# Kernel tuning notes

Hardware: AMD Instinct MI355X
Metric: run time of the kernel (lower is better)

The kernel has to match this reference:

```python
import jax, jax.numpy as jnp
import numpy as np

NUM_HEADS = 16
NHID = 64
D = NUM_HEADS * NHID  # 1024, also keys/query/values dim and out_dim
SL, BS = 2048, 32


def setup_inputs() -> dict:
    key = jax.random.key(0)
    ks = jax.random.split(key, 7)
    s = 1.0 / np.sqrt(D)
    return {
        "query": jax.random.normal(ks[0], (BS, D), jnp.float32),
        "keys": jax.random.normal(ks[1], (SL, BS, D), jnp.float32),
        "values": jax.random.normal(ks[2], (SL, BS, D), jnp.float32),
        "Wq": jax.random.normal(ks[3], (D, D), jnp.float32) * s,
        "Wk": jax.random.normal(ks[4], (D, D), jnp.float32) * s,
        "Wv": jax.random.normal(ks[5], (D, D), jnp.float32) * s,
        "Wo": jax.random.normal(ks[6], (D, D), jnp.float32) * s,
    }


def reference(query, keys, values, Wq, Wk, Wv, Wo):
    sl, bs, _ = keys.shape
    qp = query @ Wq.T                       # [bs, H*nhid]
    kp = keys @ Wk.T                        # [sl, bs, H*nhid]
    vp = values @ Wv.T                      # [sl, bs, H*nhid]
    # elementwise multiplicative score, reduced per head
    dot = (qp * kp).reshape(sl, bs, NUM_HEADS, NHID).sum(-1) / np.sqrt(NHID)
    # NOTE: original uses log_softmax (not softmax) over the sequence dim
    w = jax.nn.log_softmax(dot, axis=0)[..., None]        # [sl, bs, H, 1]
    attn = (w * vp.reshape(sl, bs, NUM_HEADS, NHID)).sum(0)  # [bs, H, nhid]
    return attn.reshape(bs, -1) @ Wo.T                     # [bs, D]
```

## Files before the change

kernel.cpp:

```cpp
#include <hip/hip_runtime.h>

#define SL  2048
#define BSZ 32
#define DIM 1024
#define NH  16
#define HD  64

typedef __attribute__((ext_vector_type(4))) float f32x4;
typedef __attribute__((ext_vector_type(8))) short s16x8;

static __device__ __forceinline__ short f2bf(float f) {
    union { float f; unsigned u; } v; v.f = f;
    unsigned r = (v.u + 0x7fffu + ((v.u >> 16) & 1u)) >> 16;
    return (short)r;
}

__global__ __launch_bounds__(256) void k_qu(const float* __restrict__ query,
                                            const float* __restrict__ Wq,
                                            const float* __restrict__ Wk,
                                            short* __restrict__ u) {
    int b = blockIdx.x & 31;
    int h = blockIdx.x >> 5;
    int t = threadIdx.x;
    __shared__ float red[256];
    __shared__ float sq[HD];
    {
        int i  = t >> 2;
        int kq = t & 3;
        const float* q = query + (size_t)b * DIM + kq * 256;
        const float* w = Wq + (size_t)(h * HD + i) * DIM + kq * 256;
        f32x4 acc = {0.f, 0.f, 0.f, 0.f};
#pragma unroll 4
        for (int k = 0; k < 256; k += 4)
            acc += *(const f32x4*)(q + k) * *(const f32x4*)(w + k);
        red[t] = acc[0] + acc[1] + acc[2] + acc[3];
    }
    __syncthreads();
    if (t < HD) sq[t] = (red[t*4] + red[t*4+1] + red[t*4+2] + red[t*4+3]) * 0.125f;
    __syncthreads();
    f32x4 acc = {0.f, 0.f, 0.f, 0.f};
    const float* wk = Wk + (size_t)(h * HD) * DIM;
#pragma unroll 8
    for (int i = 0; i < HD; ++i) {
        float s = sq[i];
        const float* row = wk + (size_t)i * DIM;
        acc[0] += s * row[t];
        acc[1] += s * row[t + 256];
        acc[2] += s * row[t + 512];
        acc[3] += s * row[t + 768];
    }
    short* ub = u + ((size_t)(b * NH + h)) * DIM;
    ub[t]       = f2bf(acc[0]);
    ub[t + 256] = f2bf(acc[1]);
    ub[t + 512] = f2bf(acc[2]);
    ub[t + 768] = f2bf(acc[3]);
}

__global__ __launch_bounds__(256, 4) void k_dot(const float* __restrict__ keys,
                                                const short* __restrict__ u,
                                                float* __restrict__ dot,
                                                float2* __restrict__ part) {
    int b  = blockIdx.x & 31;
    int st = blockIdx.x >> 5;
    int s0 = st * 64;
    __shared__ short ulds[NH][DIM + 8];
    {
        const uint4* src = (const uint4*)(u + (size_t)b * NH * DIM);
        for (int idx = threadIdx.x; idx < NH * DIM / 8; idx += 256) {
            int row = idx >> 7;
            int col = (idx & 127) * 8;
            *(uint4*)&ulds[row][col] = src[idx];
        }
    }
    __syncthreads();
    int lane = threadIdx.x & 63;
    int wave = threadIdx.x >> 6;
    int lrow = lane & 15;
    int kgrp = lane >> 4;
    f32x4 acc = {0.f, 0.f, 0.f, 0.f};
    const float* ka = keys + ((size_t)(s0 + wave * 16 + lrow) * BSZ + b) * DIM;
#pragma unroll 4
    for (int k0 = 0; k0 < DIM; k0 += 32) {
        int kj = k0 + kgrp * 8;
        s16x8 bf = *(const s16x8*)&ulds[lrow][kj];
        f32x4 a0 = *(const f32x4*)(ka + kj);
        f32x4 a1 = *(const f32x4*)(ka + kj + 4);
        s16x8 af;
        af[0]=f2bf(a0[0]); af[1]=f2bf(a0[1]); af[2]=f2bf(a0[2]); af[3]=f2bf(a0[3]);
        af[4]=f2bf(a1[0]); af[5]=f2bf(a1[1]); af[6]=f2bf(a1[2]); af[7]=f2bf(a1[3]);
        acc = __builtin_amdgcn_mfma_f32_16x16x32_bf16(af, bf, acc, 0, 0, 0);
    }
    size_t obase = ((size_t)b * SL + (s0 + wave * 16 + kgrp * 4)) * NH + lrow;
#pragma unroll
    for (int r = 0; r < 4; ++r)
        dot[obase + (size_t)r * NH] = acc[r];

    __shared__ float mred[4][16], lred[4][16];
    float m = fmaxf(fmaxf(acc[0], acc[1]), fmaxf(acc[2], acc[3]));
    m = fmaxf(m, __shfl_xor(m, 16));
    m = fmaxf(m, __shfl_xor(m, 32));
    if (lane < 16) mred[wave][lrow] = m;
    __syncthreads();
    float mb = fmaxf(fmaxf(mred[0][lrow], mred[1][lrow]),
                     fmaxf(mred[2][lrow], mred[3][lrow]));
    float l = __expf(acc[0]-mb) + __expf(acc[1]-mb) + __expf(acc[2]-mb) + __expf(acc[3]-mb);
    l += __shfl_xor(l, 16);
    l += __shfl_xor(l, 32);
    if (lane < 16) lred[wave][lrow] = l;
    __syncthreads();
    int t = threadIdx.x;
    if (t < 16) {
        float mbb = fmaxf(fmaxf(mred[0][t], mred[1][t]), fmaxf(mred[2][t], mred[3][t]));
        float lb  = lred[0][t] + lred[1][t] + lred[2][t] + lred[3][t];
        part[((size_t)b * 32 + st) * 16 + t] = make_float2(mbb, lb);
    }
}

__global__ __launch_bounds__(256, 4) void k_z(const float* __restrict__ values,
                                              const float* __restrict__ w,
                                              const float2* __restrict__ part,
                                              float* __restrict__ z) {
    int x  = blockIdx.x;
    int b  = x & 31;
    int jc = (x >> 5) & 15;
    int sh = x >> 9;
    int t  = threadIdx.x;
    int ssub = t >> 4;
    int jq = t & 15;
    int j = jc * 64 + jq * 4;
    int wv = __builtin_amdgcn_readfirstlane(t >> 6);
    int lane = t & 63;

    __shared__ float wlds[128 * 16];
    __shared__ float Tl[16];
    __shared__ f32x4 redW[4][16][16];
    __shared__ f32x4 redV[4][16];

    if (t < 16) {
        const float2* pb = part + (size_t)b * 32 * 16 + t;
        float M = -1e30f;
#pragma unroll
        for (int i = 0; i < 32; ++i) M = fmaxf(M, pb[i * 16].x);
        float L = 0.f;
#pragma unroll
        for (int i = 0; i < 32; ++i) { float2 p = pb[i * 16]; L += p.y * __expf(p.x - M); }
        Tl[t] = M + __logf(L);
    }

    f32x4 acc[NH];
#pragma unroll
    for (int h = 0; h < NH; ++h) acc[h] = (f32x4){0.f,0.f,0.f,0.f};
    f32x4 accV = {0.f,0.f,0.f,0.f};

    const float* vbase = values + (size_t)b * DIM + j;
    const float* wbase = w + ((size_t)b * SL + sh * 1024) * NH;

    const f32x4* src = (const f32x4*)wbase;
    f32x4 w0 = src[t], w1 = src[t + 256];

    for (int ph = 0; ph < 8; ++ph) {
        __syncthreads();
        f32x4* dst = (f32x4*)wlds;
        dst[t]       = w0;
        dst[t + 256] = w1;
        __syncthreads();
        if (ph + 1 < 8) {
            src += 512;
            w0 = src[t];
            w1 = src[t + 256];
        }
        int sbase = sh * 1024 + ph * 128;
#pragma unroll 4
        for (int it = 0; it < 8; ++it) {
            int s_loc = it * 16 + ssub;
            f32x4 v = *(const f32x4*)(vbase + (size_t)(sbase + s_loc) * (BSZ * DIM));
            const f32x4* wr = (const f32x4*)(wlds + s_loc * 16);
            f32x4 wv0 = wr[0], wv1 = wr[1], wv2 = wr[2], wv3 = wr[3];
            acc[0]  += v * wv0[0]; acc[1]  += v * wv0[1]; acc[2]  += v * wv0[2]; acc[3]  += v * wv0[3];
            acc[4]  += v * wv1[0]; acc[5]  += v * wv1[1]; acc[6]  += v * wv1[2]; acc[7]  += v * wv1[3];
            acc[8]  += v * wv2[0]; acc[9]  += v * wv2[1]; acc[10] += v * wv2[2]; acc[11] += v * wv2[3];
            acc[12] += v * wv3[0]; acc[13] += v * wv3[1]; acc[14] += v * wv3[2]; acc[15] += v * wv3[3];
            accV += v;
        }
    }

#pragma unroll
    for (int h = 0; h < NH; ++h) {
#pragma unroll
        for (int e = 0; e < 4; ++e) {
            float x0 = acc[h][e];
            x0 += __shfl_xor(x0, 16);
            x0 += __shfl_xor(x0, 32);
            acc[h][e] = x0;
        }
    }
#pragma unroll
    for (int e = 0; e < 4; ++e) {
        float x0 = accV[e];
        x0 += __shfl_xor(x0, 16);
        x0 += __shfl_xor(x0, 32);
        accV[e] = x0;
    }
    if (lane < 16) {
#pragma unroll
        for (int h = 0; h < NH; ++h) redW[wv][h][lane] = acc[h];
        redV[wv][lane] = accV;
    }
    __syncthreads();
    int h2 = t >> 4, q = t & 15;
    f32x4 sumW = redW[0][h2][q] + redW[1][h2][q] + redW[2][h2][q] + redW[3][h2][q];
    f32x4 sumV = redV[0][q] + redV[1][q] + redV[2][q] + redV[3][q];
    float Th = Tl[h2];
    f32x4 zv = sumW - Th * sumV;
    float* zp = z + (size_t)sh * (BSZ * NH * DIM);
    *(f32x4*)(zp + ((size_t)(b * NH + h2)) * DIM + jc * 64 + q * 4) = zv;
}

template<bool DUAL>
__global__ __launch_bounds__(256) void k_gemm(const float* __restrict__ A,
                                              const float* __restrict__ A2,
                                              const float* __restrict__ W,
                                              float* __restrict__ O,
                                              int rmul, int hsel) {
    int oc = blockIdx.x & 15;
    int b  = blockIdx.x >> 4;
    int wv = __builtin_amdgcn_readfirstlane(threadIdx.x >> 6);
    int lane = threadIdx.x & 63;
    int o = oc * 64 + lane;
    int row = b * rmul + (hsel ? oc : 0);
    const float* arow  = A + (size_t)row * DIM + wv * 256;
    const float* a2row = DUAL ? (A2 + (size_t)row * DIM + wv * 256) : nullptr;
    const float* wrow  = W + (size_t)o * DIM + wv * 256;
    f32x4 acc = {0.f, 0.f, 0.f, 0.f};
#pragma unroll 4
    for (int k = 0; k < 256; k += 4) {
        f32x4 a = *(const f32x4*)(arow + k);
        if (DUAL) a += *(const f32x4*)(a2row + k);
        f32x4 w = *(const f32x4*)(wrow + k);
        acc += a * w;
    }
    __shared__ float red[4][64];
    red[wv][lane] = acc[0] + acc[1] + acc[2] + acc[3];
    __syncthreads();
    int t = threadIdx.x;
    if (t < 64)
        O[(size_t)b * DIM + oc * 64 + t] = red[0][t] + red[1][t] + red[2][t] + red[3][t];
}

extern "C" void kernel_launch(void* const* d_in, const int* in_sizes, int n_in,
                              void* d_out, int out_size, void* d_ws, size_t ws_size,
                              hipStream_t stream) {
    const float* query  = (const float*)d_in[0];
    const float* keys   = (const float*)d_in[1];
    const float* values = (const float*)d_in[2];
    const float* Wq = (const float*)d_in[3];
    const float* Wk = (const float*)d_in[4];
    const float* Wv = (const float*)d_in[5];
    const float* Wo = (const float*)d_in[6];
    float* out = (float*)d_out;

    char* ws = (char*)d_ws;
    short*  u    = (short*)(ws + 0);
    float*  dotb = (float*)(ws + (1 << 20));
    float*  z0   = (float*)(ws + (5 << 20));
    float*  z1   = (float*)(ws + (7 << 20));
    float*  attn = (float*)(ws + (9 << 20));
    float2* part = (float2*)(ws + (9 << 20) + (128 << 10));

    hipLaunchKernelGGL(k_qu,          dim3(512),  dim3(256), 0, stream, query, Wq, Wk, u);
    hipLaunchKernelGGL(k_dot,         dim3(1024), dim3(256), 0, stream, keys, u, dotb, part);
    hipLaunchKernelGGL(k_z,           dim3(1024), dim3(256), 0, stream, values, dotb, part, z0);
    hipLaunchKernelGGL(k_gemm<true>,  dim3(512),  dim3(256), 0, stream, z0, z1, Wv, attn, 16, 1);
    hipLaunchKernelGGL(k_gemm<false>, dim3(512),  dim3(256), 0, stream, attn, nullptr, Wo, out, 1, 0);
}
```

Before: 229.4 us.

## Parallelize softmax partial reduction and drop register prefetch of weight tiles

The per-head log-sum-exp merge of 32 partials now runs in two stages: 128 threads each merge 4 partials, then 16 threads combine the 8 results through shared memory, replacing the serial 32-step loop done by 16 threads. The register double-buffered prefetch of weight tiles is removed, so each phase loads its tile directly from global memory into LDS, which lowers register pressure at the cost of exposing the load latency. The inner loop reads weights as scalars from LDS instead of four vector loads, leaving the load width to the compiler.

```diff
diff --git a/kernel.cpp b/kernel.cpp
--- a/kernel.cpp
+++ b/kernel.cpp
@@ -133,17 +133,28 @@
 
     __shared__ float wlds[128 * 16];
     __shared__ float Tl[16];
+    __shared__ float mred8[8][16], lred8[8][16];
     __shared__ f32x4 redW[4][16][16];
     __shared__ f32x4 redV[4][16];
 
+    if (t < 128) {
+        int h = t & 15, g = t >> 4;
+        const float2* pb = part + (size_t)b * 32 * 16 + h;
+        float2 p0 = pb[(g*4+0)*16], p1 = pb[(g*4+1)*16],
+               p2 = pb[(g*4+2)*16], p3 = pb[(g*4+3)*16];
+        float M = fmaxf(fmaxf(p0.x, p1.x), fmaxf(p2.x, p3.x));
+        float L = p0.y*__expf(p0.x-M) + p1.y*__expf(p1.x-M)
+                + p2.y*__expf(p2.x-M) + p3.y*__expf(p3.x-M);
+        mred8[g][h] = M; lred8[g][h] = L;
+    }
+    __syncthreads();
     if (t < 16) {
-        const float2* pb = part + (size_t)b * 32 * 16 + t;
-        float M = -1e30f;
-#pragma unroll
-        for (int i = 0; i < 32; ++i) M = fmaxf(M, pb[i * 16].x);
+        float M = mred8[0][t];
+#pragma unroll
+        for (int g = 1; g < 8; ++g) M = fmaxf(M, mred8[g][t]);
         float L = 0.f;
 #pragma unroll
-        for (int i = 0; i < 32; ++i) { float2 p = pb[i * 16]; L += p.y * __expf(p.x - M); }
+        for (int g = 0; g < 8; ++g) L += lred8[g][t] * __expf(mred8[g][t] - M);
         Tl[t] = M + __logf(L);
     }
 
@@ -155,31 +166,26 @@
     const float* vbase = values + (size_t)b * DIM + j;
     const float* wbase = w + ((size_t)b * SL + sh * 1024) * NH;
 
-    const f32x4* src = (const f32x4*)wbase;
-    f32x4 w0 = src[t], w1 = src[t + 256];
-
     for (int ph = 0; ph < 8; ++ph) {
         __syncthreads();
-        f32x4* dst = (f32x4*)wlds;
-        dst[t]       = w0;
-        dst[t + 256] = w1;
+        {
+            const f32x4* src = (const f32x4*)(wbase + ph * 128 * NH);
+            f32x4* dst = (f32x4*)wlds;
+            dst[t]       = src[t];
+            dst[t + 256] = src[t + 256];
+        }
         __syncthreads();
-        if (ph + 1 < 8) {
-            src += 512;
-            w0 = src[t];
-            w1 = src[t + 256];
-        }
         int sbase = sh * 1024 + ph * 128;
 #pragma unroll 4
         for (int it = 0; it < 8; ++it) {
             int s_loc = it * 16 + ssub;
             f32x4 v = *(const f32x4*)(vbase + (size_t)(sbase + s_loc) * (BSZ * DIM));
-            const f32x4* wr = (const f32x4*)(wlds + s_loc * 16);
-            f32x4 wv0 = wr[0], wv1 = wr[1], wv2 = wr[2], wv3 = wr[3];
-            acc[0]  += v * wv0[0]; acc[1]  += v * wv0[1]; acc[2]  += v * wv0[2]; acc[3]  += v * wv0[3];
-            acc[4]  += v * wv1[0]; acc[5]  += v * wv1[1]; acc[6]  += v * wv1[2]; acc[7]  += v * wv1[3];
-            acc[8]  += v * wv2[0]; acc[9]  += v * wv2[1]; acc[10] += v * wv2[2]; acc[11] += v * wv2[3];
-            acc[12] += v * wv3[0]; acc[13] += v * wv3[1]; acc[14] += v * wv3[2]; acc[15] += v * wv3[3];
+            const float* wr = wlds + s_loc * 16;
+#pragma unroll
+            for (int h = 0; h < NH; ++h) {
+                float wh = wr[h];
+                acc[h] += v * wh;
+            }
             accV += v;
         }
     }
```

New measurement: 207.9 us. 1.1x faster.

## Widen dot and z kernels to 512 threads, drop split-sequence z partials

Applied to the files above, without the earlier changes.

k_dot now processes 128 sequence rows per block with 8 waves, which halves the block count and the number of softmax partials. k_z no longer splits the sequence into two halves with separate z buffers. Each block instead covers the full sequence with 512 threads, each handling 2 columns instead of 4, and the DUAL sum in the first GEMM is removed. This cuts launch-level duplication and an extra z buffer pass, at the cost of longer per-block loops, fewer blocks, and the loss of the register-prefetch double buffering of the weights.

```diff
diff --git a/kernel.cpp b/kernel.cpp
--- a/kernel.cpp
+++ b/kernel.cpp
@@ -7,6 +7,7 @@
 #define HD  64
 
 typedef __attribute__((ext_vector_type(4))) float f32x4;
+typedef __attribute__((ext_vector_type(2))) float f32x2;
 typedef __attribute__((ext_vector_type(8))) short s16x8;
 
 static __device__ __forceinline__ short f2bf(float f) {
@@ -56,25 +57,29 @@
     ub[t + 768] = f2bf(acc[3]);
 }
 
-__global__ __launch_bounds__(256, 4) void k_dot(const float* __restrict__ keys,
+__global__ __launch_bounds__(512, 6) void k_dot(const float* __restrict__ keys,
                                                 const short* __restrict__ u,
                                                 float* __restrict__ dot,
                                                 float2* __restrict__ part) {
     int b  = blockIdx.x & 31;
     int st = blockIdx.x >> 5;
-    int s0 = st * 64;
+    int s0 = st * 128;
     __shared__ short ulds[NH][DIM + 8];
+    __shared__ float mred[8][16], lred[8][16];
+    int t = threadIdx.x;
     {
         const uint4* src = (const uint4*)(u + (size_t)b * NH * DIM);
-        for (int idx = threadIdx.x; idx < NH * DIM / 8; idx += 256) {
+#pragma unroll
+        for (int r = 0; r < 4; ++r) {
+            int idx = t + r * 512;
             int row = idx >> 7;
             int col = (idx & 127) * 8;
             *(uint4*)&ulds[row][col] = src[idx];
         }
     }
     __syncthreads();
-    int lane = threadIdx.x & 63;
-    int wave = threadIdx.x >> 6;
+    int lane = t & 63;
+    int wave = t >> 6;
     int lrow = lane & 15;
     int kgrp = lane >> 4;
     f32x4 acc = {0.f, 0.f, 0.f, 0.f};
@@ -95,91 +100,88 @@
     for (int r = 0; r < 4; ++r)
         dot[obase + (size_t)r * NH] = acc[r];
 
-    __shared__ float mred[4][16], lred[4][16];
     float m = fmaxf(fmaxf(acc[0], acc[1]), fmaxf(acc[2], acc[3]));
     m = fmaxf(m, __shfl_xor(m, 16));
     m = fmaxf(m, __shfl_xor(m, 32));
     if (lane < 16) mred[wave][lrow] = m;
     __syncthreads();
-    float mb = fmaxf(fmaxf(mred[0][lrow], mred[1][lrow]),
-                     fmaxf(mred[2][lrow], mred[3][lrow]));
+    float mb = mred[0][lrow];
+#pragma unroll
+    for (int w = 1; w < 8; ++w) mb = fmaxf(mb, mred[w][lrow]);
     float l = __expf(acc[0]-mb) + __expf(acc[1]-mb) + __expf(acc[2]-mb) + __expf(acc[3]-mb);
     l += __shfl_xor(l, 16);
     l += __shfl_xor(l, 32);
     if (lane < 16) lred[wave][lrow] = l;
     __syncthreads();
-    int t = threadIdx.x;
     if (t < 16) {
-        float mbb = fmaxf(fmaxf(mred[0][t], mred[1][t]), fmaxf(mred[2][t], mred[3][t]));
-        float lb  = lred[0][t] + lred[1][t] + lred[2][t] + lred[3][t];
-        part[((size_t)b * 32 + st) * 16 + t] = make_float2(mbb, lb);
-    }
-}
-
-__global__ __launch_bounds__(256, 4) void k_z(const float* __restrict__ values,
-                                              const float* __restrict__ w,
+        float mbb = mred[0][t];
+#pragma unroll
+        for (int w = 1; w < 8; ++w) mbb = fmaxf(mbb, mred[w][t]);
+        float lb = lred[0][t];
+#pragma unroll
+        for (int w = 1; w < 8; ++w) lb += lred[w][t];
+        part[((size_t)b * 16 + st) * 16 + t] = make_float2(mbb, lb);
+    }
+}
+
+__global__ __launch_bounds__(512, 6) void k_z(const float* __restrict__ values,
+                                              const float* __restrict__ dotb,
                                               const float2* __restrict__ part,
                                               float* __restrict__ z) {
-    int x  = blockIdx.x;
-    int b  = x & 31;
-    int jc = (x >> 5) & 15;
-    int sh = x >> 9;
+    int b  = blockIdx.x & 31;
+    int jc = blockIdx.x >> 5;
     int t  = threadIdx.x;
-    int ssub = t >> 4;
-    int jq = t & 15;
-    int j = jc * 64 + jq * 4;
-    int wv = __builtin_amdgcn_readfirstlane(t >> 6);
+    int ssub = t >> 5;
+    int jq   = t & 31;
+    int wave = t >> 6;
     int lane = t & 63;
 
     __shared__ float wlds[128 * 16];
     __shared__ float Tl[16];
-    __shared__ f32x4 redW[4][16][16];
-    __shared__ f32x4 redV[4][16];
+    __shared__ f32x2 redW[8][16][32];
+    __shared__ f32x2 redV[8][32];
 
     if (t < 16) {
-        const float2* pb = part + (size_t)b * 32 * 16 + t;
+        const float2* pb = part + (size_t)b * 16 * 16 + t;
         float M = -1e30f;
 #pragma unroll
-        for (int i = 0; i < 32; ++i) M = fmaxf(M, pb[i * 16].x);
+        for (int i = 0; i < 16; ++i) M = fmaxf(M, pb[i * 16].x);
         float L = 0.f;
 #pragma unroll
-        for (int i = 0; i < 32; ++i) { float2 p = pb[i * 16]; L += p.y * __expf(p.x - M); }
+        for (int i = 0; i < 16; ++i) { float2 p = pb[i * 16]; L += p.y * __expf(p.x - M); }
         Tl[t] = M + __logf(L);
     }
 
-    f32x4 acc[NH];
-#pragma unroll
-    for (int h = 0; h < NH; ++h) acc[h] = (f32x4){0.f,0.f,0.f,0.f};
-    f32x4 accV = {0.f,0.f,0.f,0.f};
-
-    const float* vbase = values + (size_t)b * DIM + j;
-    const float* wbase = w + ((size_t)b * SL + sh * 1024) * NH;
-
-    const f32x4* src = (const f32x4*)wbase;
-    f32x4 w0 = src[t], w1 = src[t + 256];
-
-    for (int ph = 0; ph < 8; ++ph) {
+    f32x2 acc[NH];
+#pragma unroll
+    for (int h = 0; h < NH; ++h) acc[h] = (f32x2){0.f, 0.f};
+    f32x2 accV = {0.f, 0.f};
+
+    const float* vbase = values + (size_t)b * DIM + jc * 64 + jq * 2;
+    const float* wbase = dotb + (size_t)b * SL * NH;
+
+    for (int ph = 0; ph < 16; ++ph) {
         __syncthreads();
-        f32x4* dst = (f32x4*)wlds;
-        dst[t]       = w0;
-        dst[t + 256] = w1;
+        {
+            const f32x4* src = (const f32x4*)(wbase + ph * 128 * NH);
+            ((f32x4*)wlds)[t] = src[t];
+        }
         __syncthreads();
-        if (ph + 1 < 8) {
-            src += 512;
-            w0 = src[t];
-            w1 = src[t + 256];
-        }
-        int sbase = sh * 1024 + ph * 128;
+        int sbase = ph * 128;
 #pragma unroll 4
         for (int it = 0; it < 8; ++it) {
             int s_loc = it * 16 + ssub;
-            f32x4 v = *(const f32x4*)(vbase + (size_t)(sbase + s_loc) * (BSZ * DIM));
+            f32x2 v = *(const f32x2*)(vbase + (size_t)(sbase + s_loc) * (BSZ * DIM));
             const f32x4* wr = (const f32x4*)(wlds + s_loc * 16);
-            f32x4 wv0 = wr[0], wv1 = wr[1], wv2 = wr[2], wv3 = wr[3];
-            acc[0]  += v * wv0[0]; acc[1]  += v * wv0[1]; acc[2]  += v * wv0[2]; acc[3]  += v * wv0[3];
-            acc[4]  += v * wv1[0]; acc[5]  += v * wv1[1]; acc[6]  += v * wv1[2]; acc[7]  += v * wv1[3];
-            acc[8]  += v * wv2[0]; acc[9]  += v * wv2[1]; acc[10] += v * wv2[2]; acc[11] += v * wv2[3];
-            acc[12] += v * wv3[0]; acc[13] += v * wv3[1]; acc[14] += v * wv3[2]; acc[15] += v * wv3[3];
+            f32x4 w0 = wr[0], w1 = wr[1], w2 = wr[2], w3 = wr[3];
+            acc[0]  += v * w0[0];  acc[1]  += v * w0[1];
+            acc[2]  += v * w0[2];  acc[3]  += v * w0[3];
+            acc[4]  += v * w1[0];  acc[5]  += v * w1[1];
+            acc[6]  += v * w1[2];  acc[7]  += v * w1[3];
+            acc[8]  += v * w2[0];  acc[9]  += v * w2[1];
+            acc[10] += v * w2[2];  acc[11] += v * w2[3];
+            acc[12] += v * w3[0];  acc[13] += v * w3[1];
+            acc[14] += v * w3[2];  acc[15] += v * w3[3];
             accV += v;
         }
     }
@@ -187,38 +189,39 @@
 #pragma unroll
     for (int h = 0; h < NH; ++h) {
 #pragma unroll
-        for (int e = 0; e < 4; ++e) {
+        for (int e = 0; e < 2; ++e) {
             float x0 = acc[h][e];
-            x0 += __shfl_xor(x0, 16);
             x0 += __shfl_xor(x0, 32);
             acc[h][e] = x0;
         }
     }
 #pragma unroll
-    for (int e = 0; e < 4; ++e) {
+    for (int e = 0; e < 2; ++e) {
         float x0 = accV[e];
-        x0 += __shfl_xor(x0, 16);
         x0 += __shfl_xor(x0, 32);
         accV[e] = x0;
     }
-    if (lane < 16) {
-#pragma unroll
-        for (int h = 0; h < NH; ++h) redW[wv][h][lane] = acc[h];
-        redV[wv][lane] = accV;
-    }
-    __syncthreads();
-    int h2 = t >> 4, q = t & 15;
-    f32x4 sumW = redW[0][h2][q] + redW[1][h2][q] + redW[2][h2][q] + redW[3][h2][q];
-    f32x4 sumV = redV[0][q] + redV[1][q] + redV[2][q] + redV[3][q];
-    float Th = Tl[h2];
-    f32x4 zv = sumW - Th * sumV;
-    float* zp = z + (size_t)sh * (BSZ * NH * DIM);
-    *(f32x4*)(zp + ((size_t)(b * NH + h2)) * DIM + jc * 64 + q * 4) = zv;
-}
-
-template<bool DUAL>
+    if (lane < 32) {
+#pragma unroll
+        for (int h = 0; h < NH; ++h) redW[wave][h][lane] = acc[h];
+        redV[wave][lane] = accV;
+    }
+    __syncthreads();
+    {
+        int h = t >> 5, q = t & 31;
+        f32x2 sumW = redW[0][h][q];
+        f32x2 sumV = redV[0][q];
+#pragma unroll
+        for (int w = 1; w < 8; ++w) { sumW += redW[w][h][q]; sumV += redV[w][q]; }
+        float Th = Tl[h];
+        float2 zv;
+        zv.x = sumW[0] - Th * sumV[0];
+        zv.y = sumW[1] - Th * sumV[1];
+        *(float2*)(z + ((size_t)(b * NH + h)) * DIM + jc * 64 + q * 2) = zv;
+    }
+}
+
 __global__ __launch_bounds__(256) void k_gemm(const float* __restrict__ A,
-                                              const float* __restrict__ A2,
                                               const float* __restrict__ W,
                                               float* __restrict__ O,
                                               int rmul, int hsel) {
@@ -228,14 +231,12 @@
     int lane = threadIdx.x & 63;
     int o = oc * 64 + lane;
     int row = b * rmul + (hsel ? oc : 0);
-    const float* arow  = A + (size_t)row * DIM + wv * 256;
-    const float* a2row = DUAL ? (A2 + (size_t)row * DIM + wv * 256) : nullptr;
-    const float* wrow  = W + (size_t)o * DIM + wv * 256;
+    const float* arow = A + (size_t)row * DIM + wv * 256;
+    const float* wrow = W + (size_t)o * DIM + wv * 256;
     f32x4 acc = {0.f, 0.f, 0.f, 0.f};
 #pragma unroll 4
     for (int k = 0; k < 256; k += 4) {
         f32x4 a = *(const f32x4*)(arow + k);
-        if (DUAL) a += *(const f32x4*)(a2row + k);
         f32x4 w = *(const f32x4*)(wrow + k);
         acc += a * w;
     }
@@ -262,14 +263,13 @@
     char* ws = (char*)d_ws;
     short*  u    = (short*)(ws + 0);
     float*  dotb = (float*)(ws + (1 << 20));
-    float*  z0   = (float*)(ws + (5 << 20));
-    float*  z1   = (float*)(ws + (7 << 20));
-    float*  attn = (float*)(ws + (9 << 20));
-    float2* part = (float2*)(ws + (9 << 20) + (128 << 10));
-
-    hipLaunchKernelGGL(k_qu,          dim3(512),  dim3(256), 0, stream, query, Wq, Wk, u);
-    hipLaunchKernelGGL(k_dot,         dim3(1024), dim3(256), 0, stream, keys, u, dotb, part);
-    hipLaunchKernelGGL(k_z,           dim3(1024), dim3(256), 0, stream, values, dotb, part, z0);
-    hipLaunchKernelGGL(k_gemm<true>,  dim3(512),  dim3(256), 0, stream, z0, z1, Wv, attn, 16, 1);
-    hipLaunchKernelGGL(k_gemm<false>, dim3(512),  dim3(256), 0, stream, attn, nullptr, Wo, out, 1, 0);
-}
+    float2* part = (float2*)(ws + (5 << 20));
+    float*  z    = (float*)(ws + (5 << 20) + (128 << 10));
+    float*  attn = (float*)(ws + (7 << 20) + (128 << 10));
+
+    hipLaunchKernelGGL(k_qu,   dim3(512), dim3(256), 0, stream, query, Wq, Wk, u);
+    hipLaunchKernelGGL(k_dot,  dim3(512), dim3(512), 0, stream, keys, u, dotb, part);
+    hipLaunchKernelGGL(k_z,    dim3(512), dim3(512), 0, stream, values, dotb, part, z);
+    hipLaunchKernelGGL(k_gemm, dim3(512), dim3(256), 0, stream, z, Wv, attn, 16, 1);
+    hipLaunchKernelGGL(k_gemm, dim3(512), dim3(256), 0, stream, attn, Wo, out, 1, 0);
+}
```

Measured after the change: 227.4 us. About the same (-0.9%).
